# Performance work log

Hardware: AMD Instinct MI355X
Metric: run time of the kernel (lower is better)

## Reference

```python
import jax, jax.numpy as jnp
import numpy as np

NPOINT = 1024
RADIUS = 0.9
NSAMPLE = 32
MLP = [64, 64, 128]
IN_CH = 67
BN_EPS = 1e-5


def setup_inputs() -> dict:
    key = jax.random.key(0)
    ks = jax.random.split(key, 2 + 2 * len(MLP))
    B, N, C = 16, 4096, 64
    inp = {}
    inp["xyz"] = jax.random.uniform(ks[0], (B, N, 3), dtype=jnp.float32)
    inp["points"] = jax.random.normal(ks[1], (B, N, C), dtype=jnp.float32)
    last = IN_CH
    for i, oc in enumerate(MLP):
        inp[f"w{i}"] = jax.random.normal(ks[2 + 2 * i], (oc, last), dtype=jnp.float32) * (1.0 / np.sqrt(last))
        inp[f"b{i}"] = jax.random.normal(ks[3 + 2 * i], (oc,), dtype=jnp.float32) * 0.01
        inp[f"g{i}"] = jnp.ones((oc,), jnp.float32)
        inp[f"beta{i}"] = jnp.zeros((oc,), jnp.float32)
        last = oc
    return inp


def _farthest_point_sample(xyz, npoint):
    # Sequential FPS; initial farthest index fixed to 0 (torch used randint) for determinism.
    B, N, _ = xyz.shape

    def step(carry, _):
        distance, far = carry
        cen = jnp.take_along_axis(xyz, far[:, None, None], axis=1)  # [B,1,3]
        d = jnp.sum((xyz - cen) ** 2, -1)                            # [B,N]
        distance = jnp.minimum(distance, d)
        new_far = jnp.argmax(distance, axis=-1).astype(jnp.int32)
        return (distance, new_far), far

    init = (jnp.full((B, N), 1e10, xyz.dtype), jnp.zeros((B,), jnp.int32))
    _, cents = jax.lax.scan(step, init, None, length=npoint)  # [npoint, B]
    return jnp.transpose(cents)  # [B, npoint]


def _gather(points, idx):
    # points [B,N,C], idx [B,S] or [B,S,K]
    return jax.vmap(lambda p, i: p[i])(points, idx)


def _query_ball_point(radius, nsample, xyz, new_xyz):
    # Faithful to source: Euclidean distance (cdist p=2) compared against radius**2.
    B, N, _ = xyz.shape
    d2 = (jnp.sum(new_xyz ** 2, -1)[:, :, None]
          + jnp.sum(xyz ** 2, -1)[:, None, :]
          - 2.0 * jnp.einsum('bsc,bnc->bsn', new_xyz, xyz))
    dist = jnp.sqrt(jnp.maximum(d2, 0.0))                  # [B,S,N]
    arang = jnp.arange(N, dtype=jnp.int32)[None, None, :]
    gi = jnp.where(dist > radius ** 2, N, arang)           # [B,S,N]
    gi = jnp.sort(gi, axis=-1)[:, :, :nsample]             # [B,S,K]
    first = gi[:, :, :1]
    gi = jnp.where(gi == N, first, gi)
    return gi


def _forward(xyz, points, params):
    idx = _farthest_point_sample(xyz, NPOINT)              # [B,S]
    new_xyz = _gather(xyz, idx)                            # [B,S,3]
    gidx = _query_ball_point(RADIUS, NSAMPLE, xyz, new_xyz)
    grouped_xyz = _gather(xyz, gidx)                       # [B,S,K,3]
    grouped_xyz_norm = grouped_xyz - new_xyz[:, :, None, :]
    grouped_pts = _gather(points, gidx)                    # [B,S,K,C]
    x = jnp.concatenate([grouped_xyz_norm, grouped_pts], axis=-1)  # [B,S,K,3+C]
    x = jnp.transpose(x, (0, 3, 1, 2))                     # [B,Cin,S,K]
    for (w, b, g, be) in params:
        x = jnp.einsum('oc,bcsk->bosk', w, x) + b[None, :, None, None]
        mu = jnp.mean(x, axis=(0, 2, 3), keepdims=True)    # BN in training mode (batch stats, biased var)
        var = jnp.mean((x - mu) ** 2, axis=(0, 2, 3), keepdims=True)
        x = (x - mu) / jnp.sqrt(var + BN_EPS) * g[None, :, None, None] + be[None, :, None, None]
        x = jax.nn.relu(x)
    new_points = jnp.max(x, axis=-1)                       # [B,Cout,S]
    new_points = jnp.transpose(new_points, (0, 2, 1))      # [B,S,Cout]
    return new_xyz, new_points


def reference(xyz, points, w0, b0, g0, beta0, w1, b1, g1, beta1, w2, b2, g2, beta2):
    params = [(w0, b0, g0, beta0), (w1, b1, g1, beta1), (w2, b2, g2, beta2)]
    return _forward(xyz, points, params)
```

## Files before the change

kernel.cpp:

```cpp
#include <hip/hip_runtime.h>
#include <hip/hip_bf16.h>
#include <stdint.h>

#define BB 16
#define NN 4096
#define NPOINT 1024
#define NSAMPLE 32

typedef unsigned int u32;
typedef unsigned long long u64;
typedef unsigned short u16;
typedef float f32x2 __attribute__((ext_vector_type(2)));
using frag_ab = __attribute__((ext_vector_type(8))) short;
using frag_cd = __attribute__((ext_vector_type(4))) float;

__device__ inline u16 f2bf(float x){ u32 u = __float_as_uint(x); u32 r = (u + 0x7fffu + ((u>>16)&1u)) >> 16; return (u16)r; }
__device__ inline float bf2f(u32 hbits){ return __uint_as_float(hbits<<16); }
__device__ inline u64 umax64(u64 a, u64 b){ return a > b ? a : b; }

__device__ inline int wave_max_bits(float v){
    int x = __float_as_int(v);
    int t;
    t = __builtin_amdgcn_update_dpp(0, x, 0x111, 0xf, 0xf, true);
    x = __float_as_int(fmaxf(__int_as_float(x), __int_as_float(t)));
    t = __builtin_amdgcn_update_dpp(0, x, 0x112, 0xf, 0xf, true);
    x = __float_as_int(fmaxf(__int_as_float(x), __int_as_float(t)));
    t = __builtin_amdgcn_update_dpp(0, x, 0x114, 0xf, 0xf, true);
    x = __float_as_int(fmaxf(__int_as_float(x), __int_as_float(t)));
    t = __builtin_amdgcn_update_dpp(0, x, 0x118, 0xf, 0xf, true);
    x = __float_as_int(fmaxf(__int_as_float(x), __int_as_float(t)));
    t = __builtin_amdgcn_update_dpp(0, x, 0x142, 0xf, 0xf, true);
    x = __float_as_int(fmaxf(__int_as_float(x), __int_as_float(t)));
    t = __builtin_amdgcn_update_dpp(0, x, 0x143, 0xf, 0xf, true);
    x = __float_as_int(fmaxf(__int_as_float(x), __int_as_float(t)));
    return __builtin_amdgcn_readlane(x, 63);
}

__global__ __launch_bounds__(256) void fps_kernel(const float* __restrict__ xyz, int* __restrict__ cents)
{
#pragma clang fp contract(off)
    __shared__ float lxyz[NN*3];
    __shared__ int lcents[NPOINT];
    __shared__ __align__(16) u64 s_red[2][4];
    const int tid = threadIdx.x;
    const int b = blockIdx.x;
    const float* gx = xyz + (size_t)b*NN*3;
    for (int i = tid; i < NN*3; i += 256) lxyz[i] = gx[i];
    __syncthreads();
    f32x2 px[8], py[8], pz[8], dist[8];
#pragma unroll
    for (int jj = 0; jj < 8; jj++){
        int p = tid*16 + jj*2;
        px[jj] = (f32x2){ lxyz[p*3+0], lxyz[(p+1)*3+0] };
        py[jj] = (f32x2){ lxyz[p*3+1], lxyz[(p+1)*3+1] };
        pz[jj] = (f32x2){ lxyz[p*3+2], lxyz[(p+1)*3+2] };
        dist[jj] = (f32x2){ 1e10f, 1e10f };
    }
    const int lane = tid & 63;
    const int wid = tid >> 6;
    int far = 0, par = 0;
    for (int s = 0; s < NPOINT; s++){
        if (tid == 0) lcents[s] = far;
        float cx = lxyz[far*3+0], cy = lxyz[far*3+1], cz = lxyz[far*3+2];
        f32x2 c2x = { cx, cx }, c2y = { cy, cy }, c2z = { cz, cz };
        float bv = -1.0f; int bj = 0;
#pragma unroll
        for (int jj = 0; jj < 8; jj++){
            f32x2 dx = px[jj] - c2x;
            f32x2 dy = py[jj] - c2y;
            f32x2 dz = pz[jj] - c2z;
            f32x2 d  = (dx*dx + dy*dy) + dz*dz;
            f32x2 nd;
            nd.x = fminf(dist[jj].x, d.x);
            nd.y = fminf(dist[jj].y, d.y);
            dist[jj] = nd;
            if (nd.x > bv){ bv = nd.x; bj = jj*2; }
            if (nd.y > bv){ bv = nd.y; bj = jj*2+1; }
        }
        int wmb = wave_max_bits(bv);
        float wmax = __int_as_float(wmb);
        u64 mask = __ballot(bv == wmax);
        int fl = __ffsll((long long)mask) - 1;
        int fj = __builtin_amdgcn_readlane(bj, fl);
        int p = (wid << 10) + (fl << 4) + fj;
        if (lane == 0) s_red[par][wid] = ((u64)(u32)wmb << 32) | (u32)(4095 - p);
        __syncthreads();
        u64 m0 = umax64(s_red[par][0], s_red[par][1]);
        u64 m1 = umax64(s_red[par][2], s_red[par][3]);
        u64 m  = umax64(m0, m1);
        far = 4095 - (int)(m & 0xFFFu);
        par ^= 1;
    }
    __syncthreads();
    for (int i = tid; i < NPOINT; i += 256) cents[b*NPOINT + i] = lcents[i];
}

__global__ __launch_bounds__(256) void gather_newxyz_kernel(const float* __restrict__ xyz, const int* __restrict__ cents,
                                                            float* __restrict__ out, float* __restrict__ nxyz)
{
    int i = blockIdx.x*256 + threadIdx.x;
    int b = i / 3072;
    int r = i - b*3072;
    int s = r / 3;
    int c = r - s*3;
    int idx = cents[b*NPOINT + s];
    float v = xyz[((size_t)b*NN + idx)*3 + c];
    out[i] = v;
    nxyz[i] = v;
}

__global__ __launch_bounds__(256) void ballquery_kernel(const float* __restrict__ xyz, const float* __restrict__ nxyz,
                                                        const int* __restrict__ cents, int* __restrict__ gidx)
{
    const int lane = threadIdx.x & 63;
    const int w = (blockIdx.x << 2) + (threadIdx.x >> 6);
    const int b = w >> 10;
    const float RAD2 = (float)(0.9*0.9);
    const float* c3 = nxyz + (size_t)w*3;
    float cx = c3[0], cy = c3[1], cz = c3[2];
    float sc = __fadd_rn(__fadd_rn(__fmul_rn(cx,cx), __fmul_rn(cy,cy)), __fmul_rn(cz,cz));
    const float* gx = xyz + (size_t)b*NN*3;
    int* gout = gidx + (size_t)w*NSAMPLE;
    int found = 0; int first = -1;
    for (int base = 0; base < NN; base += 64){
        int i = base + lane;
        float pxv = gx[i*3+0], pyv = gx[i*3+1], pzv = gx[i*3+2];
        float sp = __fadd_rn(__fadd_rn(__fmul_rn(pxv,pxv), __fmul_rn(pyv,pyv)), __fmul_rn(pzv,pzv));
        float dot = __fadd_rn(__fadd_rn(__fmul_rn(cx,pxv), __fmul_rn(cy,pyv)), __fmul_rn(cz,pzv));
        float d2 = __fsub_rn(__fadd_rn(sc, sp), __fmul_rn(2.0f, dot));
        float dd = __fsqrt_rn(fmaxf(d2, 0.0f));
        bool in = !(dd > RAD2);
        u64 m = __ballot(in);
        int cnt = __popcll(m);
        if (in){
            int slot = found + __popcll(m & ((1ull<<lane) - 1ull));
            if (slot < NSAMPLE) gout[slot] = i;
        }
        if (found == 0 && cnt > 0) first = base + (__ffsll(m) - 1);
        found += cnt;
        if (found >= NSAMPLE) break;
    }
    if (found < NSAMPLE){
        if (found == 0) first = cents[w];
        for (int slot = found + lane; slot < NSAMPLE; slot += 64) gout[slot] = first;
    }
}

__global__ __launch_bounds__(256) void conv1_kernel(const float* __restrict__ xyz, const float* __restrict__ points,
                                                    const float* __restrict__ nxyz, const int* __restrict__ gidx,
                                                    const float* __restrict__ w, const float* __restrict__ bias,
                                                    u32* __restrict__ xout, float* __restrict__ stats)
{
    __shared__ float wl[67*64];
    __shared__ float bl[64], ls[8][64], lq[8][64];
    const int tid = threadIdx.x;
    for (int i = tid; i < 67*64; i += 256){ int o = i/67, c = i - o*67; wl[c*64+o] = w[i]; }
    if (tid < 64){
        bl[tid] = bias[tid];
#pragma unroll
        for (int r = 0; r < 8; r++){ ls[r][tid] = 0.f; lq[r][tid] = 0.f; }
    }
    __syncthreads();
    const int og = tid & 3;
    const int ob = og*16;
    const int q  = tid >> 2;
    const int rp = q & 7;
    const int m0 = blockIdx.x*256 + q*4;
    const int b = m0 >> 15;
    const int s = (m0 >> 5) & 1023;
    int g[4];
#pragma unroll
    for (int i = 0; i < 4; i++) g[i] = gidx[m0+i];
    const float* c3 = nxyz + ((size_t)b*NPOINT + s)*3;
    float cx = c3[0], cy = c3[1], cz = c3[2];
    float acc[4][16];
#pragma unroll
    for (int i = 0; i < 4; i++)
#pragma unroll
        for (int o = 0; o < 16; o++) acc[i][o] = bl[ob+o];
    float fx[4], fy[4], fz[4];
#pragma unroll
    for (int i = 0; i < 4; i++){
        const float* p3 = xyz + ((size_t)b*NN + g[i])*3;
        fx[i] = p3[0]-cx; fy[i] = p3[1]-cy; fz[i] = p3[2]-cz;
    }
#pragma unroll
    for (int c = 0; c < 3; c++){
        const float* f = (c == 0) ? fx : (c == 1) ? fy : fz;
        const float* wp = &wl[c*64 + ob];
#pragma unroll
        for (int o = 0; o < 16; o++)
#pragma unroll
            for (int i = 0; i < 4; i++) acc[i][o] = fmaf(wp[o], f[i], acc[i][o]);
    }
    const float4* pr[4];
#pragma unroll
    for (int i = 0; i < 4; i++) pr[i] = (const float4*)(points + ((size_t)b*NN + g[i])*64);
#pragma unroll 4
    for (int c4 = 0; c4 < 16; c4++){
        float4 f[4];
#pragma unroll
        for (int i = 0; i < 4; i++) f[i] = pr[i][c4];
        const int cb = 3 + c4*4;
#pragma unroll
        for (int k = 0; k < 4; k++){
            const float* wp = &wl[(cb+k)*64 + ob];
#pragma unroll
            for (int o = 0; o < 16; o++){
                float wk = wp[o];
#pragma unroll
                for (int i = 0; i < 4; i++){
                    const float* fp = (const float*)&f[i];
                    acc[i][o] = fmaf(wk, fp[k], acc[i][o]);
                }
            }
        }
    }
#pragma unroll
    for (int i = 0; i < 4; i++){
        u32 tmp[8];
#pragma unroll
        for (int oo = 0; oo < 8; oo++)
            tmp[oo] = (u32)f2bf(acc[i][2*oo]) | ((u32)f2bf(acc[i][2*oo+1]) << 16);
        uint4* orow = (uint4*)(xout + (size_t)(m0+i)*32 + og*8);
        orow[0] = ((uint4*)tmp)[0];
        orow[1] = ((uint4*)tmp)[1];
    }
#pragma unroll
    for (int o = 0; o < 16; o++){
        float sv = acc[0][o]+acc[1][o]+acc[2][o]+acc[3][o];
        float qv = acc[0][o]*acc[0][o]+acc[1][o]*acc[1][o]+acc[2][o]*acc[2][o]+acc[3][o]*acc[3][o];
        atomicAdd(&ls[rp][ob+o], sv);
        atomicAdd(&lq[rp][ob+o], qv);
    }
    __syncthreads();
    if (tid < 64){
        float sm = 0.f, sq = 0.f;
#pragma unroll
        for (int r = 0; r < 8; r++){ sm += ls[r][tid]; sq += lq[r][tid]; }
        float* st = stats + (blockIdx.x & 7)*256;
        atomicAdd(&st[tid], sm);
        atomicAdd(&st[128+tid], sq);
    }
}

__device__ inline void unpack_affine_relu(uint4 u, const float* ak, const float* bk, short* dst){
    const u32* uu = (const u32*)&u;
#pragma unroll
    for (int q = 0; q < 4; q++){
        u32 v = uu[q];
        float x0 = bf2f(v & 0xffffu);
        float x1 = bf2f(v >> 16);
        float f0 = fmaxf(fmaf(ak[2*q],   x0, bk[2*q]),   0.f);
        float f1 = fmaxf(fmaf(ak[2*q+1], x1, bk[2*q+1]), 0.f);
        dst[2*q]   = (short)f2bf(f0);
        dst[2*q+1] = (short)f2bf(f1);
    }
}

__global__ __launch_bounds__(256) void conv2_kernel(const u32* __restrict__ xin, const float* __restrict__ aff,
                                                    const float* __restrict__ w, const float* __restrict__ bias,
                                                    u32* __restrict__ xout, float* __restrict__ stats)
{
    const int tid = threadIdx.x;
    const int lane = tid & 63;
    const int wid = tid >> 6;
    const int quad = lane >> 4;
    const int col = lane & 15;
    frag_ab Bf[4][2];
#pragma unroll
    for (int nt = 0; nt < 4; nt++)
#pragma unroll
        for (int kh = 0; kh < 2; kh++){
            const float* wr = w + (nt*16 + col)*64 + kh*32 + quad*8;
#pragma unroll
            for (int j = 0; j < 8; j++) Bf[nt][kh][j] = (short)f2bf(wr[j]);
        }
    float ak[2][8], bk[2][8];
#pragma unroll
    for (int kh = 0; kh < 2; kh++)
#pragma unroll
        for (int j = 0; j < 8; j++){
            int k = kh*32 + quad*8 + j;
            ak[kh][j] = aff[k]; bk[kh][j] = aff[128+k];
        }
    float biasl[4];
#pragma unroll
    for (int nt = 0; nt < 4; nt++) biasl[nt] = bias[nt*16 + col];
    float ssum[4] = {0,0,0,0}, ssq[4] = {0,0,0,0};
    u16* xo = (u16*)xout;
    const int tile0 = blockIdx.x*64 + wid*16;
    for (int t = 0; t < 16; t++){
        const size_t m0 = (size_t)(tile0 + t) * 16;
        const u32* arow = xin + (m0 + col)*32;
        uint4 u0 = *(const uint4*)(arow + quad*4);
        uint4 u1 = *(const uint4*)(arow + 16 + quad*4);
        frag_ab Af0, Af1;
        unpack_affine_relu(u0, ak[0], bk[0], (short*)&Af0);
        unpack_affine_relu(u1, ak[1], bk[1], (short*)&Af1);
        frag_cd acc[4];
#pragma unroll
        for (int nt = 0; nt < 4; nt++){
            acc[nt] = (frag_cd){biasl[nt], biasl[nt], biasl[nt], biasl[nt]};
            acc[nt] = __builtin_amdgcn_mfma_f32_16x16x32_bf16(Af0, Bf[nt][0], acc[nt], 0, 0, 0);
            acc[nt] = __builtin_amdgcn_mfma_f32_16x16x32_bf16(Af1, Bf[nt][1], acc[nt], 0, 0, 0);
        }
#pragma unroll
        for (int nt = 0; nt < 4; nt++){
#pragma unroll
            for (int r = 0; r < 4; r++){
                float v = acc[nt][r];
                xo[(m0 + quad*4 + r)*64 + nt*16 + col] = f2bf(v);
                ssum[nt] += v;
                ssq[nt] = fmaf(v, v, ssq[nt]);
            }
        }
    }
#pragma unroll
    for (int nt = 0; nt < 4; nt++){
        ssum[nt] += __shfl_xor(ssum[nt], 16); ssq[nt] += __shfl_xor(ssq[nt], 16);
        ssum[nt] += __shfl_xor(ssum[nt], 32); ssq[nt] += __shfl_xor(ssq[nt], 32);
    }
    if (quad == 0){
        float* st = stats + (blockIdx.x & 7)*256;
#pragma unroll
        for (int nt = 0; nt < 4; nt++){
            atomicAdd(&st[nt*16 + col], ssum[nt]);
            atomicAdd(&st[128 + nt*16 + col], ssq[nt]);
        }
    }
}

__global__ __launch_bounds__(256) void conv3_kernel(const u32* __restrict__ xin, const float* __restrict__ aff,
                                                    const float* __restrict__ w, const float* __restrict__ bias,
                                                    float* __restrict__ gmax, float* __restrict__ gmin,
                                                    float* __restrict__ stats)
{
    const int tid = threadIdx.x;
    const int lane = tid & 63;
    const int wid = tid >> 6;
    const int quad = lane >> 4;
    const int col = lane & 15;
    frag_ab Bf[8][2];
#pragma unroll
    for (int nt = 0; nt < 8; nt++)
#pragma unroll
        for (int kh = 0; kh < 2; kh++){
            const float* wr = w + (nt*16 + col)*64 + kh*32 + quad*8;
#pragma unroll
            for (int j = 0; j < 8; j++) Bf[nt][kh][j] = (short)f2bf(wr[j]);
        }
    float ak[2][8], bk[2][8];
#pragma unroll
    for (int kh = 0; kh < 2; kh++)
#pragma unroll
        for (int j = 0; j < 8; j++){
            int k = kh*32 + quad*8 + j;
            ak[kh][j] = aff[k]; bk[kh][j] = aff[128+k];
        }
    float biasl[8];
#pragma unroll
    for (int nt = 0; nt < 8; nt++) biasl[nt] = bias[nt*16 + col];
    float ssum[8], ssq[8], mx[8], mn[8];
#pragma unroll
    for (int nt = 0; nt < 8; nt++){ ssum[nt] = 0.f; ssq[nt] = 0.f; }
    const int tile0 = blockIdx.x*32 + wid*8;
#pragma unroll 2
    for (int t = 0; t < 8; t++){
        const size_t m0 = (size_t)(tile0 + t) * 16;
        const u32* arow = xin + (m0 + col)*32;
        uint4 u0 = *(const uint4*)(arow + quad*4);
        uint4 u1 = *(const uint4*)(arow + 16 + quad*4);
        frag_ab Af0, Af1;
        unpack_affine_relu(u0, ak[0], bk[0], (short*)&Af0);
        unpack_affine_relu(u1, ak[1], bk[1], (short*)&Af1);
        frag_cd acc[8];
#pragma unroll
        for (int nt = 0; nt < 8; nt++){
            acc[nt] = (frag_cd){biasl[nt], biasl[nt], biasl[nt], biasl[nt]};
            acc[nt] = __builtin_amdgcn_mfma_f32_16x16x32_bf16(Af0, Bf[nt][0], acc[nt], 0, 0, 0);
            acc[nt] = __builtin_amdgcn_mfma_f32_16x16x32_bf16(Af1, Bf[nt][1], acc[nt], 0, 0, 0);
        }
#pragma unroll
        for (int nt = 0; nt < 8; nt++){
            float a0 = fmaxf(fmaxf(acc[nt][0], acc[nt][1]), fmaxf(acc[nt][2], acc[nt][3]));
            float n0 = fminf(fminf(acc[nt][0], acc[nt][1]), fminf(acc[nt][2], acc[nt][3]));
            if ((t & 1) == 0){ mx[nt] = a0; mn[nt] = n0; }
            else { mx[nt] = fmaxf(mx[nt], a0); mn[nt] = fminf(mn[nt], n0); }
#pragma unroll
            for (int r = 0; r < 4; r++){
                float v = acc[nt][r];
                ssum[nt] += v;
                ssq[nt] = fmaf(v, v, ssq[nt]);
            }
        }
        if (t & 1){
#pragma unroll
            for (int nt = 0; nt < 8; nt++){
                mx[nt] = fmaxf(mx[nt], __shfl_xor(mx[nt], 16));
                mn[nt] = fminf(mn[nt], __shfl_xor(mn[nt], 16));
                mx[nt] = fmaxf(mx[nt], __shfl_xor(mx[nt], 32));
                mn[nt] = fminf(mn[nt], __shfl_xor(mn[nt], 32));
            }
            if (quad == 0){
                const int g = (tile0 + t - 1) >> 1;
#pragma unroll
                for (int nt = 0; nt < 8; nt++){
                    gmax[(size_t)g*128 + nt*16 + col] = mx[nt];
                    gmin[(size_t)g*128 + nt*16 + col] = mn[nt];
                }
            }
        }
    }
#pragma unroll
    for (int nt = 0; nt < 8; nt++){
        ssum[nt] += __shfl_xor(ssum[nt], 16); ssq[nt] += __shfl_xor(ssq[nt], 16);
        ssum[nt] += __shfl_xor(ssum[nt], 32); ssq[nt] += __shfl_xor(ssq[nt], 32);
    }
    if (quad == 0){
        float* st = stats + (blockIdx.x & 7)*256;
#pragma unroll
        for (int nt = 0; nt < 8; nt++){
            atomicAdd(&st[nt*16 + col], ssum[nt]);
            atomicAdd(&st[128 + nt*16 + col], ssq[nt]);
        }
    }
}

__global__ void finalize_kernel(const float* __restrict__ stats, const float* __restrict__ g,
                                const float* __restrict__ beta, float* __restrict__ aff, int C)
{
    int c = threadIdx.x;
    if (c < C){
        float sm = 0.f, sq = 0.f;
#pragma unroll
        for (int r = 0; r < 8; r++){ sm += stats[r*256+c]; sq += stats[r*256+128+c]; }
        const float invM = 1.0f / 524288.0f;
        float mu  = sm * invM;
        float var = fmaxf(sq * invM - mu*mu, 0.0f);
        float inv = 1.0f / sqrtf(var + 1e-5f);
        float a = g[c] * inv;
        aff[c] = a;
        aff[128+c] = beta[c] - mu*a;
    }
}

__global__ __launch_bounds__(256) void pool_kernel(const float* __restrict__ gmax, const float* __restrict__ gmin,
                                                   const float* __restrict__ aff, float* __restrict__ out)
{
    int idx = blockIdx.x*256 + threadIdx.x;
    int o = idx & 127;
    float a = aff[o], bsh = aff[128+o];
    float v = (a >= 0.f) ? fmaf(a, gmax[idx], bsh) : fmaf(a, gmin[idx], bsh);
    out[(size_t)BB*NPOINT*3 + idx] = fmaxf(v, 0.f);
}

extern "C" void kernel_launch(void* const* d_in, const int* in_sizes, int n_in,
                              void* d_out, int out_size, void* d_ws, size_t ws_size,
                              hipStream_t stream)
{
    const float* xyz    = (const float*)d_in[0];
    const float* points = (const float*)d_in[1];
    const float* w0  = (const float*)d_in[2];
    const float* b0  = (const float*)d_in[3];
    const float* g0  = (const float*)d_in[4];
    const float* be0 = (const float*)d_in[5];
    const float* w1  = (const float*)d_in[6];
    const float* b1  = (const float*)d_in[7];
    const float* g1  = (const float*)d_in[8];
    const float* be1 = (const float*)d_in[9];
    const float* w2  = (const float*)d_in[10];
    const float* b2  = (const float*)d_in[11];
    const float* g2  = (const float*)d_in[12];
    const float* be2 = (const float*)d_in[13];
    float* out = (float*)d_out;
    char* ws = (char*)d_ws;

    int*   cents = (int*)(ws + 0);
    float* nxyz  = (float*)(ws + 65536);
    int*   gidx  = (int*)(ws + 262144);
    float* stats = (float*)(ws + 2359296);
    float* aff   = (float*)(ws + 2383872);
    u32*   x1buf = (u32*)(ws + 2386944);
    u32*   x2buf = (u32*)(ws + 69495808);
    float* gmax  = (float*)(ws + 136604672);
    float* gmin  = (float*)(ws + 144993280);

    hipMemsetAsync(stats, 0, 6144*sizeof(float), stream);
    fps_kernel<<<16, 256, 0, stream>>>(xyz, cents);
    gather_newxyz_kernel<<<192, 256, 0, stream>>>(xyz, cents, out, nxyz);
    ballquery_kernel<<<4096, 256, 0, stream>>>(xyz, nxyz, cents, gidx);
    conv1_kernel<<<2048, 256, 0, stream>>>(xyz, points, nxyz, gidx, w0, b0, x1buf, stats);
    finalize_kernel<<<1, 128, 0, stream>>>(stats, g0, be0, aff, 64);
    conv2_kernel<<<512, 256, 0, stream>>>(x1buf, aff, w1, b1, x2buf, stats + 2048);
    finalize_kernel<<<1, 128, 0, stream>>>(stats + 2048, g1, be1, aff + 256, 64);
    conv3_kernel<<<1024, 256, 0, stream>>>(x2buf, aff + 256, w2, b2, gmax, gmin, stats + 4096);
    finalize_kernel<<<1, 128, 0, stream>>>(stats + 4096, g2, be2, aff + 512, 128);
    pool_kernel<<<8192, 256, 0, stream>>>(gmax, gmin, aff + 512, out);
}
```

Measured before the change: 900.2 us.

## Use bf16 MFMA in conv1, fold BN finalize into consumers, streamline FPS

Rewrites conv1 to gather pre-packed bf16 point features and compute the 64-channel part with 16x16x32 bf16 MFMA, adding the xyz offsets as scalar FMAs. A new pack kernel converts points to bf16 once, placing the buffer in the later gmax region. The separate finalize kernels are removed and each consumer recomputes BN affine parameters per block from the stats. The FPS argmax is reworked to use vector min/max with index recovery after the wave reduction, and centroids are written directly to global memory. Pool now handles eight elements per thread. Rounding point features to bf16 adds precision loss, and each block repeats the finalize work.

```diff
diff --git a/kernel.cpp b/kernel.cpp
--- a/kernel.cpp
+++ b/kernel.cpp
@@ -40,7 +40,6 @@
 {
 #pragma clang fp contract(off)
     __shared__ float lxyz[NN*3];
-    __shared__ int lcents[NPOINT];
     __shared__ __align__(16) u64 s_red[2][4];
     const int tid = threadIdx.x;
     const int b = blockIdx.x;
@@ -60,39 +59,51 @@
     const int wid = tid >> 6;
     int far = 0, par = 0;
     for (int s = 0; s < NPOINT; s++){
-        if (tid == 0) lcents[s] = far;
+        if (tid == 0) cents[b*NPOINT + s] = far;
         float cx = lxyz[far*3+0], cy = lxyz[far*3+1], cz = lxyz[far*3+2];
         f32x2 c2x = { cx, cx }, c2y = { cy, cy }, c2z = { cz, cz };
-        float bv = -1.0f; int bj = 0;
+        f32x2 bm0 = { -1.f, -1.f }, bm1 = { -1.f, -1.f };
 #pragma unroll
         for (int jj = 0; jj < 8; jj++){
             f32x2 dx = px[jj] - c2x;
             f32x2 dy = py[jj] - c2y;
             f32x2 dz = pz[jj] - c2z;
             f32x2 d  = (dx*dx + dy*dy) + dz*dz;
-            f32x2 nd;
-            nd.x = fminf(dist[jj].x, d.x);
-            nd.y = fminf(dist[jj].y, d.y);
+            f32x2 nd = __builtin_elementwise_min(dist[jj], d);
             dist[jj] = nd;
-            if (nd.x > bv){ bv = nd.x; bj = jj*2; }
-            if (nd.y > bv){ bv = nd.y; bj = jj*2+1; }
-        }
+            if (jj < 4) bm0 = __builtin_elementwise_max(bm0, nd);
+            else        bm1 = __builtin_elementwise_max(bm1, nd);
+        }
+        f32x2 bmA = __builtin_elementwise_max(bm0, bm1);
+        float bv = fmaxf(bmA.x, bmA.y);
         int wmb = wave_max_bits(bv);
         float wmax = __int_as_float(wmb);
         u64 mask = __ballot(bv == wmax);
         int fl = __ffsll((long long)mask) - 1;
-        int fj = __builtin_amdgcn_readlane(bj, fl);
-        int p = (wid << 10) + (fl << 4) + fj;
+        float g0m = fmaxf(bm0.x, bm0.y);
+        int gsel = (g0m == wmax) ? 0 : 1;
+        u32 mbits = 0;
+#pragma unroll
+        for (int u = 0; u < 4; u++){
+            f32x2 dd = gsel ? dist[4+u] : dist[u];
+            if (dd.x == wmax) mbits |= (1u << (2*u));
+            if (dd.y == wmax) mbits |= (1u << (2*u+1));
+        }
+        int fj = (gsel << 3) + (__ffs(mbits) - 1);
+        int fjw = __builtin_amdgcn_readlane(fj, fl);
+        int p = (wid << 10) + (fl << 4) + fjw;
         if (lane == 0) s_red[par][wid] = ((u64)(u32)wmb << 32) | (u32)(4095 - p);
         __syncthreads();
-        u64 m0 = umax64(s_red[par][0], s_red[par][1]);
-        u64 m1 = umax64(s_red[par][2], s_red[par][3]);
-        u64 m  = umax64(m0, m1);
+        uint4 k01 = *(const uint4*)&s_red[par][0];
+        uint4 k23 = *(const uint4*)&s_red[par][2];
+        u64 r0 = ((u64)k01.y << 32) | k01.x;
+        u64 r1 = ((u64)k01.w << 32) | k01.z;
+        u64 r2 = ((u64)k23.y << 32) | k23.x;
+        u64 r3 = ((u64)k23.w << 32) | k23.z;
+        u64 m  = umax64(umax64(r0, r1), umax64(r2, r3));
         far = 4095 - (int)(m & 0xFFFu);
         par ^= 1;
     }
-    __syncthreads();
-    for (int i = tid; i < NPOINT; i += 256) cents[b*NPOINT + i] = lcents[i];
 }
 
 __global__ __launch_bounds__(256) void gather_newxyz_kernel(const float* __restrict__ xyz, const int* __restrict__ cents,
@@ -107,6 +118,13 @@
     float v = xyz[((size_t)b*NN + idx)*3 + c];
     out[i] = v;
     nxyz[i] = v;
+}
+
+__global__ __launch_bounds__(256) void pack_points_kernel(const float* __restrict__ points, u32* __restrict__ pbf)
+{
+    int i = blockIdx.x*256 + threadIdx.x;
+    float f0 = points[2*i], f1 = points[2*i+1];
+    pbf[i] = (u32)f2bf(f0) | ((u32)f2bf(f1) << 16);
 }
 
 __global__ __launch_bounds__(256) void ballquery_kernel(const float* __restrict__ xyz, const float* __restrict__ nxyz,
@@ -146,101 +164,109 @@
     }
 }
 
-__global__ __launch_bounds__(256) void conv1_kernel(const float* __restrict__ xyz, const float* __restrict__ points,
+__global__ __launch_bounds__(256) void conv1_kernel(const float* __restrict__ xyz, const u32* __restrict__ pbf,
                                                     const float* __restrict__ nxyz, const int* __restrict__ gidx,
                                                     const float* __restrict__ w, const float* __restrict__ bias,
                                                     u32* __restrict__ xout, float* __restrict__ stats)
 {
-    __shared__ float wl[67*64];
-    __shared__ float bl[64], ls[8][64], lq[8][64];
+    __shared__ float sxyz[512][3];
     const int tid = threadIdx.x;
-    for (int i = tid; i < 67*64; i += 256){ int o = i/67, c = i - o*67; wl[c*64+o] = w[i]; }
-    if (tid < 64){
-        bl[tid] = bias[tid];
-#pragma unroll
-        for (int r = 0; r < 8; r++){ ls[r][tid] = 0.f; lq[r][tid] = 0.f; }
+    const int lane = tid & 63;
+    const int wid = tid >> 6;
+    const int quad = lane >> 4;
+    const int col = lane & 15;
+    const int blockbase = blockIdx.x*512;
+    for (int r = tid; r < 512; r += 256){
+        int m = blockbase + r;
+        int b = m >> 15, s = (m >> 5) & 1023, g = gidx[m];
+        const float* p3 = xyz + ((size_t)(b<<12) + g)*3;
+        const float* c3 = nxyz + ((size_t)b*NPOINT + s)*3;
+        sxyz[r][0] = p3[0]-c3[0]; sxyz[r][1] = p3[1]-c3[1]; sxyz[r][2] = p3[2]-c3[2];
+    }
+    frag_ab Bf[4][2];
+#pragma unroll
+    for (int nt = 0; nt < 4; nt++)
+#pragma unroll
+        for (int kh = 0; kh < 2; kh++){
+            const float* wr = w + (nt*16 + col)*67 + 3 + kh*32 + quad*8;
+#pragma unroll
+            for (int j = 0; j < 8; j++) Bf[nt][kh][j] = (short)f2bf(wr[j]);
+        }
+    float wx[4], wy[4], wz[4], biasl[4];
+#pragma unroll
+    for (int nt = 0; nt < 4; nt++){
+        const float* wb = w + (nt*16 + col)*67;
+        wx[nt] = wb[0]; wy[nt] = wb[1]; wz[nt] = wb[2];
+        biasl[nt] = bias[nt*16 + col];
     }
     __syncthreads();
-    const int og = tid & 3;
-    const int ob = og*16;
-    const int q  = tid >> 2;
-    const int rp = q & 7;
-    const int m0 = blockIdx.x*256 + q*4;
-    const int b = m0 >> 15;
-    const int s = (m0 >> 5) & 1023;
-    int g[4];
-#pragma unroll
-    for (int i = 0; i < 4; i++) g[i] = gidx[m0+i];
-    const float* c3 = nxyz + ((size_t)b*NPOINT + s)*3;
-    float cx = c3[0], cy = c3[1], cz = c3[2];
-    float acc[4][16];
-#pragma unroll
-    for (int i = 0; i < 4; i++)
-#pragma unroll
-        for (int o = 0; o < 16; o++) acc[i][o] = bl[ob+o];
-    float fx[4], fy[4], fz[4];
-#pragma unroll
-    for (int i = 0; i < 4; i++){
-        const float* p3 = xyz + ((size_t)b*NN + g[i])*3;
-        fx[i] = p3[0]-cx; fy[i] = p3[1]-cy; fz[i] = p3[2]-cz;
-    }
-#pragma unroll
-    for (int c = 0; c < 3; c++){
-        const float* f = (c == 0) ? fx : (c == 1) ? fy : fz;
-        const float* wp = &wl[c*64 + ob];
-#pragma unroll
-        for (int o = 0; o < 16; o++)
-#pragma unroll
-            for (int i = 0; i < 4; i++) acc[i][o] = fmaf(wp[o], f[i], acc[i][o]);
-    }
-    const float4* pr[4];
-#pragma unroll
-    for (int i = 0; i < 4; i++) pr[i] = (const float4*)(points + ((size_t)b*NN + g[i])*64);
-#pragma unroll 4
-    for (int c4 = 0; c4 < 16; c4++){
-        float4 f[4];
-#pragma unroll
-        for (int i = 0; i < 4; i++) f[i] = pr[i][c4];
-        const int cb = 3 + c4*4;
-#pragma unroll
-        for (int k = 0; k < 4; k++){
-            const float* wp = &wl[(cb+k)*64 + ob];
-#pragma unroll
-            for (int o = 0; o < 16; o++){
-                float wk = wp[o];
-#pragma unroll
-                for (int i = 0; i < 4; i++){
-                    const float* fp = (const float*)&f[i];
-                    acc[i][o] = fmaf(wk, fp[k], acc[i][o]);
-                }
+    float ssum[4] = {0,0,0,0}, ssq[4] = {0,0,0,0};
+    u16* xo = (u16*)xout;
+    const int tile0 = blockIdx.x*32 + wid*8;
+#pragma unroll 2
+    for (int t = 0; t < 8; t++){
+        const int tile = tile0 + t;
+        const size_t m0 = (size_t)tile * 16;
+        const int b = (int)(m0 >> 15);
+        const int g = gidx[m0 + col];
+        const u32* arow = pbf + ((size_t)(b<<12) + g)*32;
+        uint4 u0 = *(const uint4*)(arow + quad*4);
+        uint4 u1 = *(const uint4*)(arow + 16 + quad*4);
+        frag_ab Af0, Af1;
+        __builtin_memcpy(&Af0, &u0, 16);
+        __builtin_memcpy(&Af1, &u1, 16);
+        frag_cd acc[4];
+#pragma unroll
+        for (int nt = 0; nt < 4; nt++){
+            acc[nt] = (frag_cd){0.f, 0.f, 0.f, 0.f};
+            acc[nt] = __builtin_amdgcn_mfma_f32_16x16x32_bf16(Af0, Bf[nt][0], acc[nt], 0, 0, 0);
+            acc[nt] = __builtin_amdgcn_mfma_f32_16x16x32_bf16(Af1, Bf[nt][1], acc[nt], 0, 0, 0);
+        }
+        const int rbase = (int)(m0 - blockbase) + quad*4;
+#pragma unroll
+        for (int r = 0; r < 4; r++){
+            float xnx = sxyz[rbase+r][0], xny = sxyz[rbase+r][1], xnz = sxyz[rbase+r][2];
+#pragma unroll
+            for (int nt = 0; nt < 4; nt++){
+                float v = acc[nt][r] + biasl[nt];
+                v = fmaf(wx[nt], xnx, v);
+                v = fmaf(wy[nt], xny, v);
+                v = fmaf(wz[nt], xnz, v);
+                xo[(m0 + quad*4 + r)*64 + nt*16 + col] = f2bf(v);
+                ssum[nt] += v;
+                ssq[nt] = fmaf(v, v, ssq[nt]);
             }
         }
     }
 #pragma unroll
-    for (int i = 0; i < 4; i++){
-        u32 tmp[8];
-#pragma unroll
-        for (int oo = 0; oo < 8; oo++)
-            tmp[oo] = (u32)f2bf(acc[i][2*oo]) | ((u32)f2bf(acc[i][2*oo+1]) << 16);
-        uint4* orow = (uint4*)(xout + (size_t)(m0+i)*32 + og*8);
-        orow[0] = ((uint4*)tmp)[0];
-        orow[1] = ((uint4*)tmp)[1];
-    }
-#pragma unroll
-    for (int o = 0; o < 16; o++){
-        float sv = acc[0][o]+acc[1][o]+acc[2][o]+acc[3][o];
-        float qv = acc[0][o]*acc[0][o]+acc[1][o]*acc[1][o]+acc[2][o]*acc[2][o]+acc[3][o]*acc[3][o];
-        atomicAdd(&ls[rp][ob+o], sv);
-        atomicAdd(&lq[rp][ob+o], qv);
-    }
-    __syncthreads();
-    if (tid < 64){
+    for (int nt = 0; nt < 4; nt++){
+        ssum[nt] += __shfl_xor(ssum[nt], 16); ssq[nt] += __shfl_xor(ssq[nt], 16);
+        ssum[nt] += __shfl_xor(ssum[nt], 32); ssq[nt] += __shfl_xor(ssq[nt], 32);
+    }
+    if (quad == 0){
+        float* st = stats + (blockIdx.x & 7)*256;
+#pragma unroll
+        for (int nt = 0; nt < 4; nt++){
+            atomicAdd(&st[nt*16 + col], ssum[nt]);
+            atomicAdd(&st[128 + nt*16 + col], ssq[nt]);
+        }
+    }
+}
+
+__device__ inline void block_finalize(const float* __restrict__ stats, const float* __restrict__ g,
+                                      const float* __restrict__ beta, float* saff, int C, int tid)
+{
+    if (tid < C){
         float sm = 0.f, sq = 0.f;
 #pragma unroll
-        for (int r = 0; r < 8; r++){ sm += ls[r][tid]; sq += lq[r][tid]; }
-        float* st = stats + (blockIdx.x & 7)*256;
-        atomicAdd(&st[tid], sm);
-        atomicAdd(&st[128+tid], sq);
+        for (int r = 0; r < 8; r++){ sm += stats[r*256+tid]; sq += stats[r*256+128+tid]; }
+        const float invM = 1.0f / 524288.0f;
+        float mu  = sm * invM;
+        float var = fmaxf(sq * invM - mu*mu, 0.0f);
+        float inv = 1.0f / sqrtf(var + 1e-5f);
+        float a = g[tid] * inv;
+        saff[tid] = a;
+        saff[128+tid] = beta[tid] - mu*a;
     }
 }
 
@@ -258,11 +284,14 @@
     }
 }
 
-__global__ __launch_bounds__(256) void conv2_kernel(const u32* __restrict__ xin, const float* __restrict__ aff,
+__global__ __launch_bounds__(256) void conv2_kernel(const u32* __restrict__ xin, const float* __restrict__ stats_in,
+                                                    const float* __restrict__ gw, const float* __restrict__ beta,
                                                     const float* __restrict__ w, const float* __restrict__ bias,
                                                     u32* __restrict__ xout, float* __restrict__ stats)
 {
+    __shared__ float saff[256];
     const int tid = threadIdx.x;
+    block_finalize(stats_in, gw, beta, saff, 64, tid);
     const int lane = tid & 63;
     const int wid = tid >> 6;
     const int quad = lane >> 4;
@@ -276,17 +305,18 @@
 #pragma unroll
             for (int j = 0; j < 8; j++) Bf[nt][kh][j] = (short)f2bf(wr[j]);
         }
+    float biasl[4];
+#pragma unroll
+    for (int nt = 0; nt < 4; nt++) biasl[nt] = bias[nt*16 + col];
+    __syncthreads();
     float ak[2][8], bk[2][8];
 #pragma unroll
     for (int kh = 0; kh < 2; kh++)
 #pragma unroll
         for (int j = 0; j < 8; j++){
             int k = kh*32 + quad*8 + j;
-            ak[kh][j] = aff[k]; bk[kh][j] = aff[128+k];
-        }
-    float biasl[4];
-#pragma unroll
-    for (int nt = 0; nt < 4; nt++) biasl[nt] = bias[nt*16 + col];
+            ak[kh][j] = saff[k]; bk[kh][j] = saff[128+k];
+        }
     float ssum[4] = {0,0,0,0}, ssq[4] = {0,0,0,0};
     u16* xo = (u16*)xout;
     const int tile0 = blockIdx.x*64 + wid*16;
@@ -331,12 +361,15 @@
     }
 }
 
-__global__ __launch_bounds__(256) void conv3_kernel(const u32* __restrict__ xin, const float* __restrict__ aff,
+__global__ __launch_bounds__(256) void conv3_kernel(const u32* __restrict__ xin, const float* __restrict__ stats_in,
+                                                    const float* __restrict__ gw, const float* __restrict__ beta,
                                                     const float* __restrict__ w, const float* __restrict__ bias,
                                                     float* __restrict__ gmax, float* __restrict__ gmin,
                                                     float* __restrict__ stats)
 {
+    __shared__ float saff[256];
     const int tid = threadIdx.x;
+    block_finalize(stats_in, gw, beta, saff, 64, tid);
     const int lane = tid & 63;
     const int wid = tid >> 6;
     const int quad = lane >> 4;
@@ -350,17 +383,18 @@
 #pragma unroll
             for (int j = 0; j < 8; j++) Bf[nt][kh][j] = (short)f2bf(wr[j]);
         }
+    float biasl[8];
+#pragma unroll
+    for (int nt = 0; nt < 8; nt++) biasl[nt] = bias[nt*16 + col];
+    __syncthreads();
     float ak[2][8], bk[2][8];
 #pragma unroll
     for (int kh = 0; kh < 2; kh++)
 #pragma unroll
         for (int j = 0; j < 8; j++){
             int k = kh*32 + quad*8 + j;
-            ak[kh][j] = aff[k]; bk[kh][j] = aff[128+k];
-        }
-    float biasl[8];
-#pragma unroll
-    for (int nt = 0; nt < 8; nt++) biasl[nt] = bias[nt*16 + col];
+            ak[kh][j] = saff[k]; bk[kh][j] = saff[128+k];
+        }
     float ssum[8], ssq[8], mx[8], mn[8];
 #pragma unroll
     for (int nt = 0; nt < 8; nt++){ ssum[nt] = 0.f; ssq[nt] = 0.f; }
@@ -427,32 +461,23 @@
     }
 }
 
-__global__ void finalize_kernel(const float* __restrict__ stats, const float* __restrict__ g,
-                                const float* __restrict__ beta, float* __restrict__ aff, int C)
-{
-    int c = threadIdx.x;
-    if (c < C){
-        float sm = 0.f, sq = 0.f;
-#pragma unroll
-        for (int r = 0; r < 8; r++){ sm += stats[r*256+c]; sq += stats[r*256+128+c]; }
-        const float invM = 1.0f / 524288.0f;
-        float mu  = sm * invM;
-        float var = fmaxf(sq * invM - mu*mu, 0.0f);
-        float inv = 1.0f / sqrtf(var + 1e-5f);
-        float a = g[c] * inv;
-        aff[c] = a;
-        aff[128+c] = beta[c] - mu*a;
-    }
-}
-
 __global__ __launch_bounds__(256) void pool_kernel(const float* __restrict__ gmax, const float* __restrict__ gmin,
-                                                   const float* __restrict__ aff, float* __restrict__ out)
-{
-    int idx = blockIdx.x*256 + threadIdx.x;
-    int o = idx & 127;
-    float a = aff[o], bsh = aff[128+o];
-    float v = (a >= 0.f) ? fmaf(a, gmax[idx], bsh) : fmaf(a, gmin[idx], bsh);
-    out[(size_t)BB*NPOINT*3 + idx] = fmaxf(v, 0.f);
+                                                   const float* __restrict__ stats_in, const float* __restrict__ gw,
+                                                   const float* __restrict__ beta, float* __restrict__ out)
+{
+    __shared__ float saff[256];
+    const int tid = threadIdx.x;
+    block_finalize(stats_in, gw, beta, saff, 128, tid);
+    __syncthreads();
+    const int base = blockIdx.x*2048 + tid;
+#pragma unroll
+    for (int k = 0; k < 8; k++){
+        int idx = base + k*256;
+        int o = idx & 127;
+        float a = saff[o], bsh = saff[128+o];
+        float v = (a >= 0.f) ? fmaf(a, gmax[idx], bsh) : fmaf(a, gmin[idx], bsh);
+        out[(size_t)BB*NPOINT*3 + idx] = fmaxf(v, 0.f);
+    }
 }
 
 extern "C" void kernel_launch(void* const* d_in, const int* in_sizes, int n_in,
@@ -480,21 +505,19 @@
     float* nxyz  = (float*)(ws + 65536);
     int*   gidx  = (int*)(ws + 262144);
     float* stats = (float*)(ws + 2359296);
-    float* aff   = (float*)(ws + 2383872);
     u32*   x1buf = (u32*)(ws + 2386944);
     u32*   x2buf = (u32*)(ws + 69495808);
     float* gmax  = (float*)(ws + 136604672);
     float* gmin  = (float*)(ws + 144993280);
+    u32*   pbf   = (u32*)(ws + 136604672);
 
     hipMemsetAsync(stats, 0, 6144*sizeof(float), stream);
     fps_kernel<<<16, 256, 0, stream>>>(xyz, cents);
     gather_newxyz_kernel<<<192, 256, 0, stream>>>(xyz, cents, out, nxyz);
+    pack_points_kernel<<<8192, 256, 0, stream>>>(points, pbf);
     ballquery_kernel<<<4096, 256, 0, stream>>>(xyz, nxyz, cents, gidx);
-    conv1_kernel<<<2048, 256, 0, stream>>>(xyz, points, nxyz, gidx, w0, b0, x1buf, stats);
-    finalize_kernel<<<1, 128, 0, stream>>>(stats, g0, be0, aff, 64);
-    conv2_kernel<<<512, 256, 0, stream>>>(x1buf, aff, w1, b1, x2buf, stats + 2048);
-    finalize_kernel<<<1, 128, 0, stream>>>(stats + 2048, g1, be1, aff + 256, 64);
-    conv3_kernel<<<1024, 256, 0, stream>>>(x2buf, aff + 256, w2, b2, gmax, gmin, stats + 4096);
-    finalize_kernel<<<1, 128, 0, stream>>>(stats + 4096, g2, be2, aff + 512, 128);
-    pool_kernel<<<8192, 256, 0, stream>>>(gmax, gmin, aff + 512, out);
-}
+    conv1_kernel<<<1024, 256, 0, stream>>>(xyz, pbf, nxyz, gidx, w0, b0, x1buf, stats);
+    conv2_kernel<<<512, 256, 0, stream>>>(x1buf, stats, g0, be0, w1, b1, x2buf, stats + 2048);
+    conv3_kernel<<<1024, 256, 0, stream>>>(x2buf, stats + 2048, g1, be1, w2, b2, gmax, gmin, stats + 4096);
+    pool_kernel<<<1024, 256, 0, stream>>>(gmax, gmin, stats + 4096, g2, be2, out);
+}
```

Measured after the change: 803.5 us. 10.7% less time.
